# Kernel optimization log

Measured on AMD Instinct MI355X. Metric: run time of the kernel, lower is better.

The kernel has to match this reference:

```python
import jax, jax.numpy as jnp
import numpy as np

N, C_IN, C_OUT = 8192, 256, 128


def setup_inputs() -> dict:
    key = jax.random.key(0)
    k1, k2, k3, k4, k5 = jax.random.split(key, 5)
    features = jax.random.normal(k1, (N, C_IN), dtype=jnp.float32)
    wavelets = jax.random.normal(k2, (N, N), dtype=jnp.float32) / np.sqrt(N)
    wavelets_inv = jax.random.normal(k3, (N, N), dtype=jnp.float32) / np.sqrt(N)
    # xavier_uniform for weight_matrix
    limit = np.sqrt(6.0 / (C_IN + C_OUT))
    weight_matrix = jax.random.uniform(k4, (C_IN, C_OUT), dtype=jnp.float32, minval=-limit, maxval=limit)
    # filter init uniform(0.9, 1.1)
    filt = jax.random.uniform(k5, (N,), dtype=jnp.float32, minval=0.9, maxval=1.1)
    return {"features": features, "wavelets": wavelets, "wavelets_inv": wavelets_inv,
            "weight_matrix": weight_matrix, "filt": filt}


def reference(features, wavelets, wavelets_inv, weight_matrix, filt):
    # transformed = features @ W                         [N, C_out]
    transformed = jnp.matmul(features, weight_matrix)
    # right = wavelets_inv @ transformed                 [N, C_out]
    right = jnp.matmul(wavelets_inv, transformed)
    # wavelets @ diag(filt) == column-wise scale of wavelets by filt
    # (same math as torch.mm(wavelets, torch.diag(filter)) without the O(N^3) GEMM)
    scaled_right = right * filt[:, None]                 # equivalent: (wavelets * filt) @ right
    out = jnp.matmul(wavelets, scaled_right)             # [N, C_out]
    return out
```

## Files before the change

### kernel.cpp

```cpp
#include <hip/hip_runtime.h>

#define MROWS 8192
#define NCOLS 128
#define LDT 88
#define KSTEP 64
#define SPLITK 8

using f32x4  = __attribute__((ext_vector_type(4))) float;
using bf16x8 = __attribute__((ext_vector_type(8))) short;
using u32x4  = __attribute__((ext_vector_type(4))) unsigned int;
using u32x2  = __attribute__((ext_vector_type(2))) unsigned int;

__device__ __forceinline__ unsigned short f2bf(float f) {
    unsigned int u = __float_as_uint(f);
    u += 0x7fffu + ((u >> 16) & 1u);
    return (unsigned short)(u >> 16);
}
__device__ __forceinline__ unsigned int pk2(float a, float b) {
    return (unsigned int)f2bf(a) | ((unsigned int)f2bf(b) << 16);
}

template <int OUTMODE>
__global__ __launch_bounds__(256, 2) void gemm_kernel(
    const float* __restrict__ A,
    const unsigned short* __restrict__ Bt,
    void* __restrict__ out,
    int Kdim, int KC, int ldb)
{
    __shared__ __align__(16) unsigned short As[128 * LDT];
    __shared__ __align__(16) unsigned short Bs[128 * LDT];

    const int tid  = threadIdx.x;
    const int wave = tid >> 6;
    const int lane = tid & 63;
    const int lrow = lane & 15;
    const int lq   = lane >> 4;
    const int mq   = (wave & 1) * 64;
    const int nq   = (wave >> 1) * 64;
    const int m0   = blockIdx.x * 128;
    const int s    = blockIdx.y;
    const int kbase = s * KC;
    const int iters = KC >> 6;

    const int trow = tid >> 3;
    const int tk   = (tid & 7) * 8;

    f32x4 areg[4][2];
    u32x4 breg[4];

    const float*          Aptr = A  + (size_t)(m0 + trow) * Kdim + tk;
    const unsigned short* Bptr = Bt + (size_t)trow * ldb + tk;

    auto load_stage = [&](int k0) {
#pragma unroll
        for (int p = 0; p < 4; ++p) {
            const float* ap = Aptr + (size_t)(p * 32) * Kdim + k0;
            areg[p][0] = *(const f32x4*)(ap);
            areg[p][1] = *(const f32x4*)(ap + 4);
            breg[p]    = *(const u32x4*)(Bptr + (size_t)(p * 32) * ldb + k0);
        }
    };
    auto store_stage = [&]() {
#pragma unroll
        for (int p = 0; p < 4; ++p) {
            int row = trow + p * 32;
            u32x4 av;
            av.x = pk2(areg[p][0].x, areg[p][0].y);
            av.y = pk2(areg[p][0].z, areg[p][0].w);
            av.z = pk2(areg[p][1].x, areg[p][1].y);
            av.w = pk2(areg[p][1].z, areg[p][1].w);
            *(u32x4*)&As[row * LDT + tk] = av;
            *(u32x4*)&Bs[row * LDT + tk] = breg[p];
        }
    };

    f32x4 acc[4][4];
#pragma unroll
    for (int i = 0; i < 4; ++i)
#pragma unroll
        for (int j = 0; j < 4; ++j)
            acc[i][j] = {0.f, 0.f, 0.f, 0.f};

    load_stage(kbase);
    for (int it = 0; it < iters; ++it) {
        __syncthreads();
        store_stage();
        __syncthreads();
        if (it + 1 < iters) load_stage(kbase + (it + 1) * KSTEP);
#pragma unroll
        for (int kk = 0; kk < 2; ++kk) {
            const int ko = kk * 32 + lq * 8;
            bf16x8 afr[4], bfr[4];
#pragma unroll
            for (int mt = 0; mt < 4; ++mt)
                afr[mt] = *(bf16x8*)&As[(mq + mt * 16 + lrow) * LDT + ko];
#pragma unroll
            for (int nt = 0; nt < 4; ++nt)
                bfr[nt] = *(bf16x8*)&Bs[(nq + nt * 16 + lrow) * LDT + ko];
#pragma unroll
            for (int mt = 0; mt < 4; ++mt)
#pragma unroll
                for (int nt = 0; nt < 4; ++nt)
                    acc[mt][nt] = __builtin_amdgcn_mfma_f32_16x16x32_bf16(
                        afr[mt], bfr[nt], acc[mt][nt], 0, 0, 0);
        }
    }

    if (OUTMODE == 0) {
        float* P = (float*)out + (size_t)s * (MROWS * NCOLS);
#pragma unroll
        for (int mt = 0; mt < 4; ++mt) {
            int r = m0 + mq + mt * 16 + lq * 4;
#pragma unroll
            for (int nt = 0; nt < 4; ++nt) {
                int c = nq + nt * 16 + lrow;
                *(f32x4*)&P[(size_t)c * MROWS + r] = acc[mt][nt];
            }
        }
    } else if (OUTMODE == 1) {
        float* P = (float*)out + (size_t)s * (MROWS * NCOLS);
#pragma unroll
        for (int mt = 0; mt < 4; ++mt) {
            int r = m0 + mq + mt * 16 + lq * 4;
#pragma unroll
            for (int nt = 0; nt < 4; ++nt) {
                int c = nq + nt * 16 + lrow;
#pragma unroll
                for (int e = 0; e < 4; ++e)
                    P[(size_t)(r + e) * NCOLS + c] = acc[mt][nt][e];
            }
        }
    } else {
        unsigned short* Tt = (unsigned short*)out;
#pragma unroll
        for (int mt = 0; mt < 4; ++mt) {
            int r = m0 + mq + mt * 16 + lq * 4;
#pragma unroll
            for (int nt = 0; nt < 4; ++nt) {
                int c = nq + nt * 16 + lrow;
                u32x2 v;
                v.x = pk2(acc[mt][nt][0], acc[mt][nt][1]);
                v.y = pk2(acc[mt][nt][2], acc[mt][nt][3]);
                *(u32x2*)&Tt[(size_t)c * MROWS + r] = v;
            }
        }
    }
}

__global__ void convert_w(const float* __restrict__ W, unsigned short* __restrict__ Wt) {
    int idx = blockIdx.x * 256 + threadIdx.x;
    int k = idx >> 7, c = idx & 127;
    Wt[c * 256 + k] = f2bf(W[idx]);
}

__global__ void reduce2(const float* __restrict__ P, const float* __restrict__ filt,
                        unsigned short* __restrict__ Rt) {
    int idx4 = (blockIdx.x * 256 + threadIdx.x) * 4;
    f32x4 sum = {0.f, 0.f, 0.f, 0.f};
#pragma unroll
    for (int s = 0; s < SPLITK; ++s)
        sum += *(const f32x4*)&P[(size_t)s * (MROWS * NCOLS) + idx4];
    int r = idx4 & (MROWS - 1);
    f32x4 fl = *(const f32x4*)&filt[r];
    sum *= fl;
    u32x2 v;
    v.x = pk2(sum.x, sum.y);
    v.y = pk2(sum.z, sum.w);
    *(u32x2*)&Rt[idx4] = v;
}

__global__ void reduce3(const float* __restrict__ P, float* __restrict__ outp) {
    int idx4 = (blockIdx.x * 256 + threadIdx.x) * 4;
    f32x4 sum = {0.f, 0.f, 0.f, 0.f};
#pragma unroll
    for (int s = 0; s < SPLITK; ++s)
        sum += *(const f32x4*)&P[(size_t)s * (MROWS * NCOLS) + idx4];
    *(f32x4*)&outp[idx4] = sum;
}

extern "C" void kernel_launch(void* const* d_in, const int* in_sizes, int n_in,
                              void* d_out, int out_size, void* d_ws, size_t ws_size,
                              hipStream_t stream) {
    const float* features     = (const float*)d_in[0];
    const float* wavelets     = (const float*)d_in[1];
    const float* wavelets_inv = (const float*)d_in[2];
    const float* W            = (const float*)d_in[3];
    const float* filt         = (const float*)d_in[4];
    float* outp = (float*)d_out;

    char* ws = (char*)d_ws;
    float*          P  = (float*)ws;
    unsigned short* Tt = (unsigned short*)(ws + (size_t)32 * 1024 * 1024);
    unsigned short* Rt = (unsigned short*)(ws + (size_t)34 * 1024 * 1024);
    unsigned short* Wt = (unsigned short*)(ws + (size_t)36 * 1024 * 1024);

    convert_w<<<128, 256, 0, stream>>>(W, Wt);
    gemm_kernel<2><<<dim3(64, 1), 256, 0, stream>>>(features, Wt, (void*)Tt, 256, 256, 256);
    gemm_kernel<0><<<dim3(64, 8), 256, 0, stream>>>(wavelets_inv, Tt, (void*)P, 8192, 1024, 8192);
    reduce2<<<1024, 256, 0, stream>>>(P, filt, Rt);
    gemm_kernel<1><<<dim3(64, 8), 256, 0, stream>>>(wavelets, Rt, (void*)P, 8192, 1024, 8192);
    reduce3<<<1024, 256, 0, stream>>>(P, outp);
}
```

Before: 627.8 us.

## Replace split-K GEMMs with tall 32-row tiles, fusing reductions and filter scaling

```diff
diff --git a/kernel.cpp b/kernel.cpp
--- a/kernel.cpp
+++ b/kernel.cpp
@@ -2,9 +2,8 @@
 
 #define MROWS 8192
 #define NCOLS 128
-#define LDT 88
-#define KSTEP 64
-#define SPLITK 8
+#define KSTEP 128
+#define LDT   136
 
 using f32x4  = __attribute__((ext_vector_type(4))) float;
 using bf16x8 = __attribute__((ext_vector_type(8))) short;
@@ -21,129 +20,121 @@
 }
 
 template <int OUTMODE>
-__global__ __launch_bounds__(256, 2) void gemm_kernel(
+__global__ __launch_bounds__(512, 2) void gemm_tall(
     const float* __restrict__ A,
     const unsigned short* __restrict__ Bt,
     void* __restrict__ out,
-    int Kdim, int KC, int ldb)
+    const float* __restrict__ filt,
+    int Kdim, int ldb)
 {
-    __shared__ __align__(16) unsigned short As[128 * LDT];
+    __shared__ __align__(16) unsigned short As[32 * LDT];
     __shared__ __align__(16) unsigned short Bs[128 * LDT];
 
     const int tid  = threadIdx.x;
-    const int wave = tid >> 6;
     const int lane = tid & 63;
+    const int w    = tid >> 6;
+    const int wm   = (w >> 2) * 16;
+    const int wn   = (w & 3) * 32;
     const int lrow = lane & 15;
     const int lq   = lane >> 4;
-    const int mq   = (wave & 1) * 64;
-    const int nq   = (wave >> 1) * 64;
-    const int m0   = blockIdx.x * 128;
-    const int s    = blockIdx.y;
-    const int kbase = s * KC;
-    const int iters = KC >> 6;
+    const int m0   = blockIdx.x * 32;
 
-    const int trow = tid >> 3;
-    const int tk   = (tid & 7) * 8;
+    const int arow = tid >> 4;
+    const int ak   = (tid & 15) * 8;
+    const int brow = tid >> 2;
+    const int bk   = (tid & 3) * 32;
 
-    f32x4 areg[4][2];
-    u32x4 breg[4];
+    const float*          Ap = A  + (size_t)(m0 + arow) * Kdim + ak;
+    const unsigned short* Bp = Bt + (size_t)brow * ldb + bk;
 
-    const float*          Aptr = A  + (size_t)(m0 + trow) * Kdim + tk;
-    const unsigned short* Bptr = Bt + (size_t)trow * ldb + tk;
+    f32x4 a0[2], a1[2];
+    u32x4 b0[4], b1[4];
 
-    auto load_stage = [&](int k0) {
+#define LDG(a, b, k0) do { \
+        a[0] = *(const f32x4*)(Ap + (k0));      \
+        a[1] = *(const f32x4*)(Ap + (k0) + 4);  \
+        const unsigned short* bp_ = Bp + (k0);  \
+        b[0] = *(const u32x4*)(bp_);            \
+        b[1] = *(const u32x4*)(bp_ + 8);        \
+        b[2] = *(const u32x4*)(bp_ + 16);       \
+        b[3] = *(const u32x4*)(bp_ + 24);       \
+    } while (0)
+
+#define STG(a, b) do { \
+        u32x4 av_;                                   \
+        av_.x = pk2(a[0].x, a[0].y);                 \
+        av_.y = pk2(a[0].z, a[0].w);                 \
+        av_.z = pk2(a[1].x, a[1].y);                 \
+        av_.w = pk2(a[1].z, a[1].w);                 \
+        *(u32x4*)&As[arow * LDT + ak] = av_;         \
+        *(u32x4*)&Bs[brow * LDT + bk]      = b[0];   \
+        *(u32x4*)&Bs[brow * LDT + bk + 8]  = b[1];   \
+        *(u32x4*)&Bs[brow * LDT + bk + 16] = b[2];   \
+        *(u32x4*)&Bs[brow * LDT + bk + 24] = b[3];   \
+    } while (0)
+
+    f32x4 acc0 = {0.f, 0.f, 0.f, 0.f};
+    f32x4 acc1 = {0.f, 0.f, 0.f, 0.f};
+
+    auto COMPUTE = [&]() {
 #pragma unroll
-        for (int p = 0; p < 4; ++p) {
-            const float* ap = Aptr + (size_t)(p * 32) * Kdim + k0;
-            areg[p][0] = *(const f32x4*)(ap);
-            areg[p][1] = *(const f32x4*)(ap + 4);
-            breg[p]    = *(const u32x4*)(Bptr + (size_t)(p * 32) * ldb + k0);
-        }
-    };
-    auto store_stage = [&]() {
-#pragma unroll
-        for (int p = 0; p < 4; ++p) {
-            int row = trow + p * 32;
-            u32x4 av;
-            av.x = pk2(areg[p][0].x, areg[p][0].y);
-            av.y = pk2(areg[p][0].z, areg[p][0].w);
-            av.z = pk2(areg[p][1].x, areg[p][1].y);
-            av.w = pk2(areg[p][1].z, areg[p][1].w);
-            *(u32x4*)&As[row * LDT + tk] = av;
-            *(u32x4*)&Bs[row * LDT + tk] = breg[p];
+        for (int kk = 0; kk < 4; ++kk) {
+            const int ko = kk * 32 + lq * 8;
+            bf16x8 af  = *(bf16x8*)&As[(wm + lrow) * LDT + ko];
+            bf16x8 bf0 = *(bf16x8*)&Bs[(wn + lrow) * LDT + ko];
+            bf16x8 bf1 = *(bf16x8*)&Bs[(wn + 16 + lrow) * LDT + ko];
+            acc0 = __builtin_amdgcn_mfma_f32_16x16x32_bf16(af, bf0, acc0, 0, 0, 0);
+            acc1 = __builtin_amdgcn_mfma_f32_16x16x32_bf16(af, bf1, acc1, 0, 0, 0);
         }
     };
 
-    f32x4 acc[4][4];
-#pragma unroll
-    for (int i = 0; i < 4; ++i)
-#pragma unroll
-        for (int j = 0; j < 4; ++j)
-            acc[i][j] = {0.f, 0.f, 0.f, 0.f};
+    const int iters = Kdim / KSTEP;
+    LDG(a0, b0, 0);
+    LDG(a1, b1, KSTEP);
+    STG(a0, b0);
+    __syncthreads();
 
-    load_stage(kbase);
-    for (int it = 0; it < iters; ++it) {
+    for (int it = 0; it < iters; it += 2) {
+        if (it + 2 < iters) LDG(a0, b0, (it + 2) * KSTEP);
+        COMPUTE();
         __syncthreads();
-        store_stage();
+        STG(a1, b1);
         __syncthreads();
-        if (it + 1 < iters) load_stage(kbase + (it + 1) * KSTEP);
-#pragma unroll
-        for (int kk = 0; kk < 2; ++kk) {
-            const int ko = kk * 32 + lq * 8;
-            bf16x8 afr[4], bfr[4];
-#pragma unroll
-            for (int mt = 0; mt < 4; ++mt)
-                afr[mt] = *(bf16x8*)&As[(mq + mt * 16 + lrow) * LDT + ko];
-#pragma unroll
-            for (int nt = 0; nt < 4; ++nt)
-                bfr[nt] = *(bf16x8*)&Bs[(nq + nt * 16 + lrow) * LDT + ko];
-#pragma unroll
-            for (int mt = 0; mt < 4; ++mt)
-#pragma unroll
-                for (int nt = 0; nt < 4; ++nt)
-                    acc[mt][nt] = __builtin_amdgcn_mfma_f32_16x16x32_bf16(
-                        afr[mt], bfr[nt], acc[mt][nt], 0, 0, 0);
+        if (it + 3 < iters) LDG(a1, b1, (it + 3) * KSTEP);
+        COMPUTE();
+        if (it + 2 < iters) {
+            __syncthreads();
+            STG(a0, b0);
+            __syncthreads();
         }
     }
+#undef LDG
+#undef STG
 
-    if (OUTMODE == 0) {
-        float* P = (float*)out + (size_t)s * (MROWS * NCOLS);
+    const int r = m0 + wm + lq * 4;
+    if (OUTMODE == 2) {
+        float* O = (float*)out;
 #pragma unroll
-        for (int mt = 0; mt < 4; ++mt) {
-            int r = m0 + mq + mt * 16 + lq * 4;
+        for (int nt = 0; nt < 2; ++nt) {
+            const int c = wn + nt * 16 + lrow;
+            const f32x4 v = nt ? acc1 : acc0;
 #pragma unroll
-            for (int nt = 0; nt < 4; ++nt) {
-                int c = nq + nt * 16 + lrow;
-                *(f32x4*)&P[(size_t)c * MROWS + r] = acc[mt][nt];
-            }
-        }
-    } else if (OUTMODE == 1) {
-        float* P = (float*)out + (size_t)s * (MROWS * NCOLS);
-#pragma unroll
-        for (int mt = 0; mt < 4; ++mt) {
-            int r = m0 + mq + mt * 16 + lq * 4;
-#pragma unroll
-            for (int nt = 0; nt < 4; ++nt) {
-                int c = nq + nt * 16 + lrow;
-#pragma unroll
-                for (int e = 0; e < 4; ++e)
-                    P[(size_t)(r + e) * NCOLS + c] = acc[mt][nt][e];
-            }
+            for (int e = 0; e < 4; ++e)
+                O[(size_t)(r + e) * NCOLS + c] = v[e];
         }
     } else {
-        unsigned short* Tt = (unsigned short*)out;
-#pragma unroll
-        for (int mt = 0; mt < 4; ++mt) {
-            int r = m0 + mq + mt * 16 + lq * 4;
-#pragma unroll
-            for (int nt = 0; nt < 4; ++nt) {
-                int c = nq + nt * 16 + lrow;
-                u32x2 v;
-                v.x = pk2(acc[mt][nt][0], acc[mt][nt][1]);
-                v.y = pk2(acc[mt][nt][2], acc[mt][nt][3]);
-                *(u32x2*)&Tt[(size_t)c * MROWS + r] = v;
-            }
+        unsigned short* O = (unsigned short*)out;
+        f32x4 v0 = acc0, v1 = acc1;
+        if (OUTMODE == 1) {
+            const f32x4 fl = *(const f32x4*)&filt[r];
+            v0 *= fl;
+            v1 *= fl;
         }
+        u32x2 o;
+        o.x = pk2(v0.x, v0.y); o.y = pk2(v0.z, v0.w);
+        *(u32x2*)&O[(size_t)(wn + lrow) * MROWS + r] = o;
+        o.x = pk2(v1.x, v1.y); o.y = pk2(v1.z, v1.w);
+        *(u32x2*)&O[(size_t)(wn + 16 + lrow) * MROWS + r] = o;
     }
 }
 
@@ -151,31 +142,6 @@
     int idx = blockIdx.x * 256 + threadIdx.x;
     int k = idx >> 7, c = idx & 127;
     Wt[c * 256 + k] = f2bf(W[idx]);
-}
-
-__global__ void reduce2(const float* __restrict__ P, const float* __restrict__ filt,
-                        unsigned short* __restrict__ Rt) {
-    int idx4 = (blockIdx.x * 256 + threadIdx.x) * 4;
-    f32x4 sum = {0.f, 0.f, 0.f, 0.f};
-#pragma unroll
-    for (int s = 0; s < SPLITK; ++s)
-        sum += *(const f32x4*)&P[(size_t)s * (MROWS * NCOLS) + idx4];
-    int r = idx4 & (MROWS - 1);
-    f32x4 fl = *(const f32x4*)&filt[r];
-    sum *= fl;
-    u32x2 v;
-    v.x = pk2(sum.x, sum.y);
-    v.y = pk2(sum.z, sum.w);
-    *(u32x2*)&Rt[idx4] = v;
-}
-
-__global__ void reduce3(const float* __restrict__ P, float* __restrict__ outp) {
-    int idx4 = (blockIdx.x * 256 + threadIdx.x) * 4;
-    f32x4 sum = {0.f, 0.f, 0.f, 0.f};
-#pragma unroll
-    for (int s = 0; s < SPLITK; ++s)
-        sum += *(const f32x4*)&P[(size_t)s * (MROWS * NCOLS) + idx4];
-    *(f32x4*)&outp[idx4] = sum;
 }
 
 extern "C" void kernel_launch(void* const* d_in, const int* in_sizes, int n_in,
@@ -189,15 +155,12 @@
     float* outp = (float*)d_out;
 
     char* ws = (char*)d_ws;
-    float*          P  = (float*)ws;
-    unsigned short* Tt = (unsigned short*)(ws + (size_t)32 * 1024 * 1024);
-    unsigned short* Rt = (unsigned short*)(ws + (size_t)34 * 1024 * 1024);
-    unsigned short* Wt = (unsigned short*)(ws + (size_t)36 * 1024 * 1024);
+    unsigned short* Tt = (unsigned short*)ws;
+    unsigned short* Rt = (unsigned short*)(ws + (size_t)2 * 1024 * 1024);
+    unsigned short* Wt = (unsigned short*)(ws + (size_t)4 * 1024 * 1024);
 
     convert_w<<<128, 256, 0, stream>>>(W, Wt);
-    gemm_kernel<2><<<dim3(64, 1), 256, 0, stream>>>(features, Wt, (void*)Tt, 256, 256, 256);
-    gemm_kernel<0><<<dim3(64, 8), 256, 0, stream>>>(wavelets_inv, Tt, (void*)P, 8192, 1024, 8192);
-    reduce2<<<1024, 256, 0, stream>>>(P, filt, Rt);
-    gemm_kernel<1><<<dim3(64, 8), 256, 0, stream>>>(wavelets, Rt, (void*)P, 8192, 1024, 8192);
-    reduce3<<<1024, 256, 0, stream>>>(P, outp);
+    gemm_tall<0><<<256, 512, 0, stream>>>(features,     Wt, (void*)Tt,   nullptr, 256,  256);
+    gemm_tall<1><<<256, 512, 0, stream>>>(wavelets_inv, Tt, (void*)Rt,   filt,    8192, 8192);
+    gemm_tall<2><<<256, 512, 0, stream>>>(wavelets,     Rt, (void*)outp, nullptr, 8192, 8192);
 }
```

Measured after the change: 585.3 us. -6.8%, faster.
